# Kernel tuning notes

Hardware: AMD Instinct MI355X
Metric: run time of the kernel (lower is better)

## Reference

```python
import jax, jax.numpy as jnp
import numpy as np
from jax import lax

D_MODEL = 512
D_INNER = 1024   # expand=2
D_STATE = 16
D_CONV = 4
DT_RANK = 32     # ceil(d_model/16)
D_FFN = 2048
EPS = 1e-6


def _layernorm(x, g, b):
    mu = jnp.mean(x, axis=-1, keepdims=True)
    var = jnp.mean((x - mu) ** 2, axis=-1, keepdims=True)
    return (x - mu) * lax.rsqrt(var + EPS) * g + b


def _mamba(x, in_w, conv_w, conv_b, xproj_w, dt_w, dt_b, A_log, D_vec, out_w):
    # x: [B, L, d_model]
    B, L, _ = x.shape
    xz = jnp.einsum('bld,ed->ble', x, in_w)           # [B, L, 2*d_inner]
    xc, z = xz[..., :D_INNER], xz[..., D_INNER:]
    # causal depthwise conv over time
    xt = xc.transpose(0, 2, 1)                        # [B, d_inner, L]
    kern = conv_w[:, None, :]                         # [d_inner, 1, d_conv]
    xt = lax.conv_general_dilated(xt, kern, (1,), [(D_CONV - 1, 0)],
                                  feature_group_count=D_INNER)
    xc = jax.nn.silu(xt.transpose(0, 2, 1) + conv_b)  # [B, L, d_inner]
    # input-dependent SSM parameters
    x_dbl = jnp.einsum('bld,ed->ble', xc, xproj_w)    # [B, L, dt_rank+2*d_state]
    dt = x_dbl[..., :DT_RANK]
    Bm = x_dbl[..., DT_RANK:DT_RANK + D_STATE]
    Cm = x_dbl[..., DT_RANK + D_STATE:]
    delta = jax.nn.softplus(jnp.einsum('blr,dr->bld', dt, dt_w) + dt_b)  # [B, L, d_inner]
    A = -jnp.exp(A_log)                               # [d_inner, d_state]

    def step(h, inp):
        d_t, u_t, b_t, c_t = inp                      # [B,di],[B,di],[B,ds],[B,ds]
        dA = jnp.exp(d_t[:, :, None] * A)             # [B, di, ds]
        dBu = (d_t * u_t)[:, :, None] * b_t[:, None, :]
        h = dA * h + dBu
        y = jnp.einsum('bds,bs->bd', h, c_t)
        return h, y

    h0 = jnp.zeros((B, D_INNER, D_STATE), x.dtype)
    xs = (delta.transpose(1, 0, 2), xc.transpose(1, 0, 2),
          Bm.transpose(1, 0, 2), Cm.transpose(1, 0, 2))
    _, ys = lax.scan(step, h0, xs)                    # [L, B, d_inner]
    y = ys.transpose(1, 0, 2) + xc * D_vec
    y = y * jax.nn.silu(z)
    return jnp.einsum('ble,de->bld', y, out_w)        # [B, L, d_model]


def setup_inputs() -> dict:
    key = jax.random.key(0)
    ks = iter(jax.random.split(key, 40))
    B, S, T = 8, 512, 1024

    def nrm(shape, scale=0.02):
        return jax.random.normal(next(ks), shape, dtype=jnp.float32) * scale

    def mamba_params(prefix):
        A_log = jnp.log(jnp.broadcast_to(jnp.arange(1, D_STATE + 1, dtype=jnp.float32),
                                         (D_INNER, D_STATE)))
        return {
            prefix + '_in_w': nrm((2 * D_INNER, D_MODEL)),
            prefix + '_conv_w': nrm((D_INNER, D_CONV), 0.1),
            prefix + '_conv_b': jnp.zeros((D_INNER,), jnp.float32),
            prefix + '_xproj_w': nrm((DT_RANK + 2 * D_STATE, D_INNER)),
            prefix + '_dt_w': nrm((D_INNER, DT_RANK), 0.1),
            prefix + '_dt_b': jnp.full((D_INNER,), -4.0, jnp.float32),
            prefix + '_A_log': A_log,
            prefix + '_D_vec': jnp.ones((D_INNER,), jnp.float32),
            prefix + '_out_w': nrm((D_MODEL, D_INNER)),
        }

    inp = {
        'tgt': jax.random.normal(next(ks), (B, S, D_MODEL), dtype=jnp.float32),
        'memory': jax.random.normal(next(ks), (B, T, D_MODEL), dtype=jnp.float32),
    }
    inp.update(mamba_params('self'))
    inp.update(mamba_params('cross'))
    inp.update({
        'ln1_g': jnp.ones((D_MODEL,), jnp.float32), 'ln1_b': jnp.zeros((D_MODEL,), jnp.float32),
        'ln2_g': jnp.ones((D_MODEL,), jnp.float32), 'ln2_b': jnp.zeros((D_MODEL,), jnp.float32),
        'ln3_g': jnp.ones((D_MODEL,), jnp.float32), 'ln3_b': jnp.zeros((D_MODEL,), jnp.float32),
        'ffn_w1': nrm((D_FFN, D_MODEL)), 'ffn_b1': jnp.zeros((D_FFN,), jnp.float32),
        'ffn_w2': nrm((D_MODEL, D_FFN)), 'ffn_b2': jnp.zeros((D_MODEL,), jnp.float32),
    })
    return inp


def reference(tgt, memory,
              self_in_w, self_conv_w, self_conv_b, self_xproj_w, self_dt_w, self_dt_b,
              self_A_log, self_D_vec, self_out_w,
              cross_in_w, cross_conv_w, cross_conv_b, cross_xproj_w, cross_dt_w, cross_dt_b,
              cross_A_log, cross_D_vec, cross_out_w,
              ln1_g, ln1_b, ln2_g, ln2_b, ln3_g, ln3_b,
              ffn_w1, ffn_b1, ffn_w2, ffn_b2):
    S = tgt.shape[1]
    # self-Mamba block (post-norm, dropout=0)
    t2 = _mamba(tgt, self_in_w, self_conv_w, self_conv_b, self_xproj_w,
                self_dt_w, self_dt_b, self_A_log, self_D_vec, self_out_w)
    t = _layernorm(tgt + t2, ln1_g, ln1_b)
    # cross-Mamba: scan over [memory; tgt], keep last S steps
    cat = jnp.concatenate([memory, t], axis=1)
    c2 = _mamba(cat, cross_in_w, cross_conv_w, cross_conv_b, cross_xproj_w,
                cross_dt_w, cross_dt_b, cross_A_log, cross_D_vec, cross_out_w)[:, -S:]
    t = _layernorm(t + c2, ln2_g, ln2_b)
    # positionwise FFN
    f = jnp.einsum('bld,fd->blf', t, ffn_w1) + ffn_b1
    f = jax.nn.relu(f)
    f = jnp.einsum('blf,df->bld', f, ffn_w2) + ffn_b2
    t = _layernorm(t + f, ln3_g, ln3_b)
    return t
```

## Files before the change

kernel.cpp:

```cpp
#include <hip/hip_runtime.h>
#include <math.h>

#define DM    512
#define DI    1024
#define DSN   16
#define DTR   32
#define DFFN  2048
#define BB    8
#define SS    512
#define TTM   1024
#define LCAT  1536
#define NC    64

#define ACT_NONE     0
#define ACT_RELU     1
#define ACT_DELTA    3
#define ACT_XDBL     4

typedef __attribute__((ext_vector_type(8))) short short8;
typedef __attribute__((ext_vector_type(8))) unsigned short ushort8;
typedef __attribute__((ext_vector_type(4))) float f32x4;

#define L2E 1.4426950408889634f

__device__ __forceinline__ unsigned short f2b(float f) {
    unsigned int u = __float_as_uint(f);
    return (unsigned short)((u + 0x7FFFu + ((u >> 16) & 1u)) >> 16);
}
__device__ __forceinline__ float b2f(unsigned short h) {
    return __uint_as_float(((unsigned int)h) << 16);
}
__device__ __forceinline__ float fast_softplus(float v) {
    return (v > 20.f) ? v : __logf(1.f + __expf(v));
}
__device__ __forceinline__ float fexp2(float x) {
#if __has_builtin(__builtin_amdgcn_exp2f)
    return __builtin_amdgcn_exp2f(x);
#else
    float r; asm("v_exp_f32 %0, %1" : "=v"(r) : "v"(x)); return r;
#endif
}
__device__ __forceinline__ float frcp(float x) {
    return __builtin_amdgcn_rcpf(x);
}
__device__ __forceinline__ void gld16(const void* g, void* l) {
    __builtin_amdgcn_global_load_lds(
        (const __attribute__((address_space(1))) void*)g,
        (__attribute__((address_space(3))) void*)l, 16, 0, 0);
}

__device__ __forceinline__ int map_row(int m, int mb, int bs, int ro) {
    int q = m / mb;
    return q * bs + ro + (m - q * mb);
}

__global__ __launch_bounds__(256) void mgemm_kernel(
    const unsigned short* __restrict__ A, int mb, int bs, int ro,
    const unsigned short* __restrict__ W, const float* __restrict__ bias,
    float* __restrict__ Cf, unsigned short* __restrict__ Cb,
    float* __restrict__ C2, float* __restrict__ Cf2,
    int N, int K, int act)
{
    __shared__ __align__(16) unsigned short As[128 * 64];
    __shared__ __align__(16) unsigned short Bs[128 * 64];
    int tid = threadIdx.x;
    int lane = tid & 63, wave = tid >> 6;
    int wy = wave >> 1, wx = wave & 1;
    int nx = gridDim.x;
    int f = blockIdx.y * nx + blockIdx.x;
    int xcd = f & 7, j2 = f >> 3;
    int bandh = gridDim.y >> 3;
    int m0 = (xcd * bandh + j2 / nx) * 128;
    int n0 = (j2 % nx) * 128;
    int Kh = K / gridDim.z;
    int kbeg = blockIdx.z * Kh, kend = kbeg + Kh;
    float* Cfo = Cf;
    const float* biaso = bias;
    if (blockIdx.z) { Cfo = Cf2; biaso = nullptr; }

    const unsigned short* ga[4];
    const unsigned short* gb[4];
    unsigned short* la[4];
    unsigned short* lb[4];
    #pragma unroll
    for (int j = 0; j < 4; j++) {
        int c  = wave * 256 + j * 64 + lane;
        int r  = c >> 3;
        int q  = c & 7;
        int g  = (q & 4) | ((q & 3) ^ (r & 3));
        int arow = map_row(m0 + r, mb, bs, ro);
        ga[j] = A + (size_t)arow * K + g * 8;
        gb[j] = W + (size_t)(n0 + r) * K + g * 8;
        la[j] = As + (size_t)(wave * 256 + j * 64) * 8;
        lb[j] = Bs + (size_t)(wave * 256 + j * 64) * 8;
    }
    int fm = lane & 15, fg = lane >> 4;
    int sw = fg ^ (fm & 3);
    const unsigned short* arp = As + ((size_t)(wy * 64 + fm) * 8 + sw) * 8;
    const unsigned short* brp = Bs + ((size_t)(wx * 64 + fm) * 8 + sw) * 8;

    f32x4 acc[4][4];
    #pragma unroll
    for (int i = 0; i < 4; i++)
        #pragma unroll
        for (int j = 0; j < 4; j++) acc[i][j] = 0.f;

    for (int k0 = kbeg; k0 < kend; k0 += 64) {
        #pragma unroll
        for (int j = 0; j < 4; j++) {
            gld16(ga[j] + k0, la[j]);
            gld16(gb[j] + k0, lb[j]);
        }
        __syncthreads();
        #pragma unroll
        for (int h = 0; h < 2; h++) {
            short8 af[4], bfr[4];
            #pragma unroll
            for (int t = 0; t < 4; t++) af[t]  = *(const short8*)(arp + h * 32 + t * 1024);
            #pragma unroll
            for (int t = 0; t < 4; t++) bfr[t] = *(const short8*)(brp + h * 32 + t * 1024);
            #pragma unroll
            for (int i = 0; i < 4; i++)
                #pragma unroll
                for (int j = 0; j < 4; j++)
                    acc[i][j] = __builtin_amdgcn_mfma_f32_16x16x32_bf16(af[i], bfr[j], acc[i][j], 0, 0, 0);
        }
        __syncthreads();
    }

    int en = lane & 15, em = (lane >> 4) * 4;
    if (act == ACT_XDBL) {
        #pragma unroll
        for (int j = 0; j < 4; j++) {
            int n = n0 + wx * 64 + j * 16 + en;
            if (n >= 64) continue;
            #pragma unroll
            for (int i = 0; i < 4; i++) {
                int mbase = m0 + wy * 64 + i * 16 + em;
                #pragma unroll
                for (int r = 0; r < 4; r++) {
                    float v = acc[i][j][r];
                    int m = mbase + r;
                    if (n < 32) {
                        Cb[(size_t)m * 64 + n] = f2b(v);
                    } else {
                        C2[(size_t)m * 32 + (n - 32)] = v;
                        Cb[(size_t)m * 64 + n] = 0;
                    }
                }
            }
        }
        return;
    }
    if (act == ACT_DELTA) {
        #pragma unroll
        for (int j = 0; j < 4; j++) {
            int n = n0 + wx * 64 + j * 16 + en;
            float bv = bias[n];
            #pragma unroll
            for (int i = 0; i < 4; i++) {
                int mbase = m0 + wy * 64 + i * 16 + em;
                #pragma unroll
                for (int r = 0; r < 4; r++) {
                    float v = acc[i][j][r] + bv;
                    Cb[(size_t)(mbase + r) * 1024 + n] = f2b(fast_softplus(v));
                }
            }
        }
        return;
    }
    #pragma unroll
    for (int j = 0; j < 4; j++) {
        int n = n0 + wx * 64 + j * 16 + en;
        float bv = biaso ? biaso[n] : 0.f;
        #pragma unroll
        for (int i = 0; i < 4; i++) {
            int mbase = m0 + wy * 64 + i * 16 + em;
            #pragma unroll
            for (int r = 0; r < 4; r++) {
                float v = acc[i][j][r] + bv;
                if (act == ACT_RELU) v = v > 0.f ? v : 0.f;
                size_t off = (size_t)(mbase + r) * N + n;
                if (Cb) Cb[off] = f2b(v);
                else    Cfo[off] = v;
            }
        }
    }
}

__global__ void xprojb_fill(const float* __restrict__ xproj, unsigned short* __restrict__ out)
{
    int idx = blockIdx.x * 256 + threadIdx.x;
    if (idx >= 131072) return;
    int n = idx >> 10;
    out[idx] = (n < 64) ? f2b(xproj[idx]) : (unsigned short)0;
}
__global__ void dtwb_fill(const float* __restrict__ dt_w, unsigned short* __restrict__ out)
{
    int idx = blockIdx.x * 256 + threadIdx.x;
    if (idx >= 65536) return;
    int n = idx >> 6, c = idx & 63;
    out[idx] = (c < 32) ? f2b(dt_w[n * 32 + c]) : (unsigned short)0;
}

__global__ __launch_bounds__(256) void conv_silu_kernel(
    const unsigned short* __restrict__ xz,
    const float* __restrict__ cw,
    const float* __restrict__ cb,
    unsigned short* __restrict__ xc, int L, int total8)
{
    int idx = blockIdx.x * blockDim.x + threadIdx.x;
    if (idx >= total8) return;
    int d8 = idx & 127;
    int d0 = d8 * 8;
    int r  = idx >> 7;
    int l  = r % L;
    float acc[8];
    {
        float4 c0 = ((const float4*)(cb + d0))[0];
        float4 c1 = ((const float4*)(cb + d0))[1];
        acc[0]=c0.x; acc[1]=c0.y; acc[2]=c0.z; acc[3]=c0.w;
        acc[4]=c1.x; acc[5]=c1.y; acc[6]=c1.z; acc[7]=c1.w;
    }
    float4 wv[8];
    #pragma unroll
    for (int j = 0; j < 8; j++) wv[j] = *(const float4*)(cw + (d0 + j) * 4);
    #pragma unroll
    for (int k = 0; k < 4; k++) {
        int ls = l - 3 + k;
        if (ls >= 0) {
            ushort8 v = *(const ushort8*)(xz + (size_t)(r - 3 + k) * 2048 + d0);
            const float* w = (const float*)&wv[0];
            #pragma unroll
            for (int j = 0; j < 8; j++)
                acc[j] = fmaf(b2f(v[j]), w[j * 4 + k], acc[j]);
        }
    }
    ushort8 o;
    #pragma unroll
    for (int j = 0; j < 8; j++) {
        float s = acc[j] * frcp(1.f + __expf(-acc[j]));
        o[j] = f2b(s);
    }
    *(ushort8*)(xc + (size_t)r * 1024 + d0) = o;
}

__global__ __launch_bounds__(256) void scan_part1(
    const unsigned short* __restrict__ delta, const unsigned short* __restrict__ xc,
    const float* __restrict__ bc, const float* __restrict__ A_log,
    float* __restrict__ part_h, float* __restrict__ part_s, int L, int CH)
{
    int tid = threadIdx.x;
    int dblk = blockIdx.x & 3;
    int c    = (blockIdx.x >> 2) & (NC - 1);
    int b    = blockIdx.x / (4 * NC);
    int d    = dblk * 256 + tid;
    float A2[DSN];
    {
        const float4* ap = (const float4*)(A_log + d * DSN);
        #pragma unroll
        for (int q = 0; q < 4; q++) {
            float4 a4 = ap[q];
            A2[q*4+0] = -__expf(a4.x) * L2E;
            A2[q*4+1] = -__expf(a4.y) * L2E;
            A2[q*4+2] = -__expf(a4.z) * L2E;
            A2[q*4+3] = -__expf(a4.w) * L2E;
        }
    }
    float h[DSN];
    #pragma unroll
    for (int s = 0; s < DSN; s++) h[s] = 0.f;
    float ssum = 0.f;
    int l0 = c * CH;
    for (int l = l0; l < l0 + CH; l++) {
        size_t r = (size_t)b * L + l;
        float4 bq[4];
        const float4* bp = (const float4*)(bc + r * 32);
        #pragma unroll
        for (int q = 0; q < 4; q++) bq[q] = bp[q];
        const float* Bm = (const float*)&bq[0];
        float dl = b2f(delta[r * DI + d]);
        float u  = b2f(xc[r * DI + d]);
        float du = dl * u;
        ssum += dl;
        #pragma unroll
        for (int s = 0; s < DSN; s++)
            h[s] = fmaf(fexp2(dl * A2[s]), h[s], du * Bm[s]);
    }
    size_t base = ((size_t)(b * NC + c) * DI + d) * DSN;
    #pragma unroll
    for (int q = 0; q < 4; q++)
        ((float4*)(part_h + base))[q] = make_float4(h[q*4], h[q*4+1], h[q*4+2], h[q*4+3]);
    part_s[(size_t)(b * NC + c) * DI + d] = ssum;
}

__global__ __launch_bounds__(256) void scan_combine(
    const float* __restrict__ A_log,
    float* __restrict__ part_h, const float* __restrict__ part_s)
{
    int idx = blockIdx.x * 256 + threadIdx.x;
    int s  = idx & (DSN - 1);
    int dd = (idx >> 4) & (DI - 1);
    int b  = idx >> 14;
    float A2 = -__expf(A_log[dd * DSN + s]) * L2E;
    float h = 0.f;
    size_t sbase = (size_t)b * NC * DI + dd;
    size_t hbase = ((size_t)b * NC * DI + dd) * DSN + s;
    for (int c = 0; c < NC; c++) {
        float ph = part_h[hbase];
        float S  = part_s[sbase];
        part_h[hbase] = h;
        h = fmaf(fexp2(A2 * S), h, ph);
        hbase += (size_t)DI * DSN;
        sbase += DI;
    }
}

__global__ __launch_bounds__(256) void scan_part2(
    const unsigned short* __restrict__ delta, const unsigned short* __restrict__ xc,
    const float* __restrict__ bc, const unsigned short* __restrict__ xz,
    const float* __restrict__ A_log, const float* __restrict__ Dv,
    const float* __restrict__ part_h,
    unsigned short* __restrict__ out, int L, int CH)
{
    int tid = threadIdx.x;
    int dblk = blockIdx.x & 3;
    int c    = (blockIdx.x >> 2) & (NC - 1);
    int b    = blockIdx.x / (4 * NC);
    int d    = dblk * 256 + tid;
    float A2[DSN];
    {
        const float4* ap = (const float4*)(A_log + d * DSN);
        #pragma unroll
        for (int q = 0; q < 4; q++) {
            float4 a4 = ap[q];
            A2[q*4+0] = -__expf(a4.x) * L2E;
            A2[q*4+1] = -__expf(a4.y) * L2E;
            A2[q*4+2] = -__expf(a4.z) * L2E;
            A2[q*4+3] = -__expf(a4.w) * L2E;
        }
    }
    float Dvd = Dv[d];
    size_t base = ((size_t)(b * NC + c) * DI + d) * DSN;
    float h4[4][4];
    #pragma unroll
    for (int q = 0; q < 4; q++) *((float4*)h4[q]) = ((const float4*)(part_h + base))[q];
    float h[DSN];
    #pragma unroll
    for (int s = 0; s < DSN; s++) h[s] = h4[s >> 2][s & 3];
    int l0 = c * CH;
    for (int l = l0; l < l0 + CH; l++) {
        size_t r = (size_t)b * L + l;
        float4 bq[8];
        const float4* bp = (const float4*)(bc + r * 32);
        #pragma unroll
        for (int q = 0; q < 8; q++) bq[q] = bp[q];
        const float* Bm = (const float*)&bq[0];
        const float* Cm = Bm + DSN;
        float dl = b2f(delta[r * DI + d]);
        float u  = b2f(xc[r * DI + d]);
        float du = dl * u;
        float y = 0.f;
        #pragma unroll
        for (int s = 0; s < DSN; s++) {
            h[s] = fmaf(fexp2(dl * A2[s]), h[s], du * Bm[s]);
            y = fmaf(h[s], Cm[s], y);
        }
        float z = b2f(xz[r * 2048 + DI + d]);
        float sil = z * frcp(1.f + __expf(-z));
        out[r * DI + d] = f2b((y + u * Dvd) * sil);
    }
}

__global__ __launch_bounds__(128) void addln_kernel(
    const float* __restrict__ a, int amb, int absd, int aro, int lda,
    const float* __restrict__ bsrc, const float* __restrict__ bsrc2,
    const float* __restrict__ g, const float* __restrict__ be,
    float* __restrict__ outf, int omb, int obsd, int oro, int ldo,
    unsigned short* __restrict__ outb, int bmb, int bbsd, int bro, int ldb)
{
    int m = blockIdx.x, t = threadIdx.x;
    int ar = map_row(m, amb, absd, aro);
    float4 x4 = ((const float4*)(a + (size_t)ar * lda))[t];
    float4 y4 = ((const float4*)(bsrc + (size_t)m * DM))[t];
    float v[4] = {x4.x + y4.x, x4.y + y4.y, x4.z + y4.z, x4.w + y4.w};
    if (bsrc2) {
        float4 z4 = ((const float4*)(bsrc2 + (size_t)m * DM))[t];
        v[0] += z4.x; v[1] += z4.y; v[2] += z4.z; v[3] += z4.w;
    }
    float sum = v[0] + v[1] + v[2] + v[3];
    float sq  = v[0]*v[0] + v[1]*v[1] + v[2]*v[2] + v[3]*v[3];
    #pragma unroll
    for (int o = 32; o > 0; o >>= 1) {
        sum += __shfl_down(sum, o);
        sq  += __shfl_down(sq, o);
    }
    __shared__ float s0[2], s1[2];
    if ((t & 63) == 0) { s0[t >> 6] = sum; s1[t >> 6] = sq; }
    __syncthreads();
    float tot = s0[0] + s0[1];
    float tsq = s1[0] + s1[1];
    float mu = tot * (1.f / DM);
    float var = tsq * (1.f / DM) - mu * mu;
    float rs = rsqrtf(var + 1e-6f);
    float4 g4 = ((const float4*)g)[t];
    float4 b4 = ((const float4*)be)[t];
    float o0 = (v[0] - mu) * rs * g4.x + b4.x;
    float o1 = (v[1] - mu) * rs * g4.y + b4.y;
    float o2 = (v[2] - mu) * rs * g4.z + b4.z;
    float o3 = (v[3] - mu) * rs * g4.w + b4.w;
    if (outf) {
        int orow = map_row(m, omb, obsd, oro);
        ((float4*)(outf + (size_t)orow * ldo))[t] = make_float4(o0, o1, o2, o3);
    }
    if (outb) {
        int brow = map_row(m, bmb, bbsd, bro);
        ((ushort4*)(outb + (size_t)brow * ldb))[t] =
            make_ushort4(f2b(o0), f2b(o1), f2b(o2), f2b(o3));
    }
}

__global__ void f2b_kernel(const float* __restrict__ in, unsigned short* __restrict__ out, int n4)
{
    int i = blockIdx.x * 256 + threadIdx.x;
    if (i >= n4) return;
    float4 v = ((const float4*)in)[i];
    ((ushort4*)out)[i] = make_ushort4(f2b(v.x), f2b(v.y), f2b(v.z), f2b(v.w));
}

struct W6 { const float* p[6]; };
__global__ void wconv_kernel(W6 w, unsigned short* __restrict__ out)
{
    const int cum[7] = {0, 262144, 524288, 655360, 786432, 1048576, 1310720};
    int i = blockIdx.x * 256 + threadIdx.x;
    if (i >= 1310720) return;
    int seg = 0;
    #pragma unroll
    for (int s = 1; s < 6; s++) seg += (i >= cum[s]);
    float4 v = ((const float4*)w.p[seg])[i - cum[seg]];
    ((ushort4*)out)[i] = make_ushort4(f2b(v.x), f2b(v.y), f2b(v.z), f2b(v.w));
}

__global__ void mem2catb_kernel(const float* __restrict__ mem, unsigned short* __restrict__ catb)
{
    int f = blockIdx.x * blockDim.x + threadIdx.x;
    const int total = BB * TTM * DM / 4;
    if (f >= total) return;
    const int per_b = TTM * DM / 4;
    int b = f / per_b, rem = f - b * per_b;
    float4 v = ((const float4*)mem)[f];
    ((ushort4*)catb)[(size_t)b * (LCAT * DM / 4) + rem] =
        make_ushort4(f2b(v.x), f2b(v.y), f2b(v.z), f2b(v.w));
}

static void run_scan(const unsigned short* dltb, const unsigned short* xcb, const float* bc,
                     const unsigned short* xzb, const float* A_log, const float* Dv,
                     float* part_h, float* part_s, unsigned short* out, int L,
                     hipStream_t stream)
{
    int CH = L / NC;
    int blocks = BB * NC * (DI / 256);
    scan_part1<<<blocks, 256, 0, stream>>>(dltb, xcb, bc, A_log, part_h, part_s, L, CH);
    scan_combine<<<BB * DI * DSN / 256, 256, 0, stream>>>(A_log, part_h, part_s);
    scan_part2<<<blocks, 256, 0, stream>>>(dltb, xcb, bc, xzb, A_log, Dv, part_h, out, L, CH);
}

extern "C" void kernel_launch(void* const* d_in, const int* in_sizes, int n_in,
                              void* d_out, int out_size, void* d_ws, size_t ws_size,
                              hipStream_t stream)
{
    const float* tgt       = (const float*)d_in[0];
    const float* memory    = (const float*)d_in[1];
    const float* s_in_w    = (const float*)d_in[2];
    const float* s_conv_w  = (const float*)d_in[3];
    const float* s_conv_b  = (const float*)d_in[4];
    const float* s_xproj_w = (const float*)d_in[5];
    const float* s_dt_w    = (const float*)d_in[6];
    const float* s_dt_b    = (const float*)d_in[7];
    const float* s_A_log   = (const float*)d_in[8];
    const float* s_D_vec   = (const float*)d_in[9];
    const float* s_out_w   = (const float*)d_in[10];
    const float* c_in_w    = (const float*)d_in[11];
    const float* c_conv_w  = (const float*)d_in[12];
    const float* c_conv_b  = (const float*)d_in[13];
    const float* c_xproj_w = (const float*)d_in[14];
    const float* c_dt_w    = (const float*)d_in[15];
    const float* c_dt_b    = (const float*)d_in[16];
    const float* c_A_log   = (const float*)d_in[17];
    const float* c_D_vec   = (const float*)d_in[18];
    const float* c_out_w   = (const float*)d_in[19];
    const float* ln1_g     = (const float*)d_in[20];
    const float* ln1_b     = (const float*)d_in[21];
    const float* ln2_g     = (const float*)d_in[22];
    const float* ln2_b     = (const float*)d_in[23];
    const float* ln3_g     = (const float*)d_in[24];
    const float* ln3_b     = (const float*)d_in[25];
    const float* ffn_w1    = (const float*)d_in[26];
    const float* ffn_b1    = (const float*)d_in[27];
    const float* ffn_w2    = (const float*)d_in[28];
    const float* ffn_b2    = (const float*)d_in[29];
    float* outp = (float*)d_out;

    float* ws     = (float*)d_ws;
    float* bc     = ws;
    float* t1     = bc     + 393216;
    float* tbuf   = t1     + 2097152;
    float* part_h = tbuf   + 2097152;
    float* proj   = part_h;
    float* proj2  = part_h + 2097152;
    float* part_s = part_h + 8388608;
    unsigned short* ub      = (unsigned short*)(part_s + 524288);
    unsigned short* dltb    = ub;
    unsigned short* catb    = dltb    + 12582912;
    unsigned short* tgtb    = catb    + 6291456;
    unsigned short* xzb     = tgtb    + 2097152;
    unsigned short* xcb     = xzb     + 25165824;
    unsigned short* ygb     = xcb     + 12582912;
    unsigned short* tbbf    = ygb     + 12582912;
    unsigned short* s_in_wb = tbbf    + 2097152;
    unsigned short* c_in_wb = s_in_wb + 1048576;
    unsigned short* s_out_wb= c_in_wb + 1048576;
    unsigned short* c_out_wb= s_out_wb+ 524288;
    unsigned short* w1b     = c_out_wb+ 524288;
    unsigned short* w2b     = w1b     + 1048576;
    unsigned short* xprojb_s= w2b     + 1048576;
    unsigned short* xprojb_c= xprojb_s+ 131072;
    unsigned short* dtwb_s  = xprojb_c+ 131072;
    unsigned short* dtwb_c  = dtwb_s  + 65536;
    unsigned short* dtb     = dtwb_c  + 65536;
    unsigned short* fbuf    = xzb;
    float* ffnout  = (float*)dltb;
    float* ffnout2 = ffnout + 2097152;

    f2b_kernel<<<(2097152/4 + 255)/256, 256, 0, stream>>>(tgt, tgtb, 2097152/4);
    mem2catb_kernel<<<(BB*TTM*DM/4 + 255)/256, 256, 0, stream>>>(memory, catb);
    {
        W6 w; w.p[0]=s_in_w; w.p[1]=c_in_w; w.p[2]=s_out_w; w.p[3]=c_out_w; w.p[4]=ffn_w1; w.p[5]=ffn_w2;
        wconv_kernel<<<(1310720 + 255)/256, 256, 0, stream>>>(w, s_in_wb);
    }
    xprojb_fill<<<131072/256, 256, 0, stream>>>(s_xproj_w, xprojb_s);
    xprojb_fill<<<131072/256, 256, 0, stream>>>(c_xproj_w, xprojb_c);
    dtwb_fill<<<65536/256, 256, 0, stream>>>(s_dt_w, dtwb_s);
    dtwb_fill<<<65536/256, 256, 0, stream>>>(c_dt_w, dtwb_c);

    mgemm_kernel<<<dim3(2048/128, 4096/128), 256, 0, stream>>>(
        tgtb, 4096, 0, 0, s_in_wb, nullptr, nullptr, xzb, nullptr, nullptr, 2048, 512, ACT_NONE);
    conv_silu_kernel<<<(BB*SS*DI/8 + 255)/256, 256, 0, stream>>>(xzb, s_conv_w, s_conv_b, xcb, SS, BB*SS*DI/8);
    mgemm_kernel<<<dim3(1, 4096/128), 256, 0, stream>>>(
        xcb, 4096, 0, 0, xprojb_s, nullptr, nullptr, dtb, bc, nullptr, 128, 1024, ACT_XDBL);
    mgemm_kernel<<<dim3(1024/128, 4096/128), 256, 0, stream>>>(
        dtb, 4096, 0, 0, dtwb_s, s_dt_b, nullptr, dltb, nullptr, nullptr, 1024, 64, ACT_DELTA);
    run_scan(dltb, xcb, bc, xzb, s_A_log, s_D_vec, part_h, part_s, ygb, SS, stream);
    mgemm_kernel<<<dim3(512/128, 4096/128, 2), 256, 0, stream>>>(
        ygb, 4096, 0, 0, s_out_wb, nullptr, proj, nullptr, nullptr, proj2, 512, 1024, ACT_NONE);
    addln_kernel<<<4096, 128, 0, stream>>>(
        tgt, 4096, 0, 0, DM, proj, proj2, ln1_g, ln1_b,
        t1, 4096, 0, 0, DM, catb, 512, 1536, 1024, DM);

    mgemm_kernel<<<dim3(2048/128, 12288/128), 256, 0, stream>>>(
        catb, 12288, 0, 0, c_in_wb, nullptr, nullptr, xzb, nullptr, nullptr, 2048, 512, ACT_NONE);
    conv_silu_kernel<<<(BB*LCAT*DI/8 + 255)/256, 256, 0, stream>>>(xzb, c_conv_w, c_conv_b, xcb, LCAT, BB*LCAT*DI/8);
    mgemm_kernel<<<dim3(1, 12288/128), 256, 0, stream>>>(
        xcb, 12288, 0, 0, xprojb_c, nullptr, nullptr, dtb, bc, nullptr, 128, 1024, ACT_XDBL);
    mgemm_kernel<<<dim3(1024/128, 12288/128), 256, 0, stream>>>(
        dtb, 12288, 0, 0, dtwb_c, c_dt_b, nullptr, dltb, nullptr, nullptr, 1024, 64, ACT_DELTA);
    run_scan(dltb, xcb, bc, xzb, c_A_log, c_D_vec, part_h, part_s, ygb, LCAT, stream);
    mgemm_kernel<<<dim3(512/128, 4096/128, 2), 256, 0, stream>>>(
        ygb, 512, 1536, 1024, c_out_wb, nullptr, proj, nullptr, nullptr, proj2, 512, 1024, ACT_NONE);
    addln_kernel<<<4096, 128, 0, stream>>>(
        t1, 4096, 0, 0, DM, proj, proj2, ln2_g, ln2_b,
        tbuf, 4096, 0, 0, DM, tbbf, 4096, 0, 0, DM);

    mgemm_kernel<<<dim3(2048/128, 4096/128), 256, 0, stream>>>(
        tbbf, 4096, 0, 0, w1b, ffn_b1, nullptr, fbuf, nullptr, nullptr, 2048, 512, ACT_RELU);
    mgemm_kernel<<<dim3(512/128, 4096/128, 2), 256, 0, stream>>>(
        fbuf, 4096, 0, 0, w2b, ffn_b2, ffnout, nullptr, nullptr, ffnout2, 512, 2048, ACT_NONE);
    addln_kernel<<<4096, 128, 0, stream>>>(
        tbuf, 4096, 0, 0, DM, ffnout, ffnout2, ln3_g, ln3_b,
        outp, 4096, 0, 0, DM, nullptr, 0, 0, 0, 0);
}
```

Before: 591.5 us.

## Skip unneeded cross-Mamba z projection and scan output for memory rows

The cross-Mamba in-projection is split in two. The x half is computed for all concatenated rows, and the z (gate) half is computed only for the last 512 rows per batch, using a new row-mapped output addressing in the GEMM. The scan's second pass now launches only the chunks that cover the kept tail (from chunk 42 on) and writes gated outputs only for positions at or after 1024. This removes GEMM and scan work whose results are discarded by the final slice, at the cost of an extra GEMM launch and some index arithmetic in the epilogue.

Measured after the change: 581.3 us. About the same (-1.7%).

```diff
diff --git a/kernel.cpp b/kernel.cpp
--- a/kernel.cpp
+++ b/kernel.cpp
@@ -59,7 +59,8 @@
     const unsigned short* __restrict__ W, const float* __restrict__ bias,
     float* __restrict__ Cf, unsigned short* __restrict__ Cb,
     float* __restrict__ C2, float* __restrict__ Cf2,
-    int N, int K, int act)
+    int N, int K, int act,
+    int omb, int obs, int oro, int ldc, int nofs)
 {
     __shared__ __align__(16) unsigned short As[128 * 64];
     __shared__ __align__(16) unsigned short Bs[128 * 64];
@@ -180,7 +181,8 @@
             for (int r = 0; r < 4; r++) {
                 float v = acc[i][j][r] + bv;
                 if (act == ACT_RELU) v = v > 0.f ? v : 0.f;
-                size_t off = (size_t)(mbase + r) * N + n;
+                int orow = map_row(mbase + r, omb, obs, oro);
+                size_t off = (size_t)orow * ldc + nofs + n;
                 if (Cb) Cb[off] = f2b(v);
                 else    Cfo[off] = v;
             }
@@ -321,12 +323,14 @@
     const float* __restrict__ bc, const unsigned short* __restrict__ xz,
     const float* __restrict__ A_log, const float* __restrict__ Dv,
     const float* __restrict__ part_h,
-    unsigned short* __restrict__ out, int L, int CH)
+    unsigned short* __restrict__ out, int L, int CH, int c0, int lmin)
 {
     int tid = threadIdx.x;
     int dblk = blockIdx.x & 3;
-    int c    = (blockIdx.x >> 2) & (NC - 1);
-    int b    = blockIdx.x / (4 * NC);
+    int rest = blockIdx.x >> 2;
+    int ncp  = NC - c0;
+    int c    = c0 + rest % ncp;
+    int b    = rest / ncp;
     int d    = dblk * 256 + tid;
     float A2[DSN];
     {
@@ -366,9 +370,11 @@
             h[s] = fmaf(fexp2(dl * A2[s]), h[s], du * Bm[s]);
             y = fmaf(h[s], Cm[s], y);
         }
-        float z = b2f(xz[r * 2048 + DI + d]);
-        float sil = z * frcp(1.f + __expf(-z));
-        out[r * DI + d] = f2b((y + u * Dvd) * sil);
+        if (l >= lmin) {
+            float z = b2f(xz[r * 2048 + DI + d]);
+            float sil = z * frcp(1.f + __expf(-z));
+            out[r * DI + d] = f2b((y + u * Dvd) * sil);
+        }
     }
 }
 
@@ -456,13 +462,14 @@
 static void run_scan(const unsigned short* dltb, const unsigned short* xcb, const float* bc,
                      const unsigned short* xzb, const float* A_log, const float* Dv,
                      float* part_h, float* part_s, unsigned short* out, int L,
-                     hipStream_t stream)
+                     int c0, int lmin, hipStream_t stream)
 {
     int CH = L / NC;
-    int blocks = BB * NC * (DI / 256);
-    scan_part1<<<blocks, 256, 0, stream>>>(dltb, xcb, bc, A_log, part_h, part_s, L, CH);
+    int blocks1 = BB * NC * (DI / 256);
+    scan_part1<<<blocks1, 256, 0, stream>>>(dltb, xcb, bc, A_log, part_h, part_s, L, CH);
     scan_combine<<<BB * DI * DSN / 256, 256, 0, stream>>>(A_log, part_h, part_s);
-    scan_part2<<<blocks, 256, 0, stream>>>(dltb, xcb, bc, xzb, A_log, Dv, part_h, out, L, CH);
+    int blocks2 = BB * (NC - c0) * (DI / 256);
+    scan_part2<<<blocks2, 256, 0, stream>>>(dltb, xcb, bc, xzb, A_log, Dv, part_h, out, L, CH, c0, lmin);
 }
 
 extern "C" void kernel_launch(void* const* d_in, const int* in_sizes, int n_in,
@@ -544,37 +551,50 @@
     dtwb_fill<<<65536/256, 256, 0, stream>>>(c_dt_w, dtwb_c);
 
     mgemm_kernel<<<dim3(2048/128, 4096/128), 256, 0, stream>>>(
-        tgtb, 4096, 0, 0, s_in_wb, nullptr, nullptr, xzb, nullptr, nullptr, 2048, 512, ACT_NONE);
+        tgtb, 4096, 0, 0, s_in_wb, nullptr, nullptr, xzb, nullptr, nullptr, 2048, 512, ACT_NONE,
+        4096, 0, 0, 2048, 0);
     conv_silu_kernel<<<(BB*SS*DI/8 + 255)/256, 256, 0, stream>>>(xzb, s_conv_w, s_conv_b, xcb, SS, BB*SS*DI/8);
     mgemm_kernel<<<dim3(1, 4096/128), 256, 0, stream>>>(
-        xcb, 4096, 0, 0, xprojb_s, nullptr, nullptr, dtb, bc, nullptr, 128, 1024, ACT_XDBL);
+        xcb, 4096, 0, 0, xprojb_s, nullptr, nullptr, dtb, bc, nullptr, 128, 1024, ACT_XDBL,
+        4096, 0, 0, 128, 0);
     mgemm_kernel<<<dim3(1024/128, 4096/128), 256, 0, stream>>>(
-        dtb, 4096, 0, 0, dtwb_s, s_dt_b, nullptr, dltb, nullptr, nullptr, 1024, 64, ACT_DELTA);
-    run_scan(dltb, xcb, bc, xzb, s_A_log, s_D_vec, part_h, part_s, ygb, SS, stream);
+        dtb, 4096, 0, 0, dtwb_s, s_dt_b, nullptr, dltb, nullptr, nullptr, 1024, 64, ACT_DELTA,
+        4096, 0, 0, 1024, 0);
+    run_scan(dltb, xcb, bc, xzb, s_A_log, s_D_vec, part_h, part_s, ygb, SS, 0, 0, stream);
     mgemm_kernel<<<dim3(512/128, 4096/128, 2), 256, 0, stream>>>(
-        ygb, 4096, 0, 0, s_out_wb, nullptr, proj, nullptr, nullptr, proj2, 512, 1024, ACT_NONE);
+        ygb, 4096, 0, 0, s_out_wb, nullptr, proj, nullptr, nullptr, proj2, 512, 1024, ACT_NONE,
+        4096, 0, 0, 512, 0);
     addln_kernel<<<4096, 128, 0, stream>>>(
         tgt, 4096, 0, 0, DM, proj, proj2, ln1_g, ln1_b,
         t1, 4096, 0, 0, DM, catb, 512, 1536, 1024, DM);
 
-    mgemm_kernel<<<dim3(2048/128, 12288/128), 256, 0, stream>>>(
-        catb, 12288, 0, 0, c_in_wb, nullptr, nullptr, xzb, nullptr, nullptr, 2048, 512, ACT_NONE);
+    mgemm_kernel<<<dim3(1024/128, 12288/128), 256, 0, stream>>>(
+        catb, 12288, 0, 0, c_in_wb, nullptr, nullptr, xzb, nullptr, nullptr, 2048, 512, ACT_NONE,
+        12288, 0, 0, 2048, 0);
+    mgemm_kernel<<<dim3(1024/128, 4096/128), 256, 0, stream>>>(
+        catb, 512, 1536, 1024, c_in_wb + 1024 * 512, nullptr, nullptr, xzb, nullptr, nullptr, 2048, 512, ACT_NONE,
+        512, 1536, 1024, 2048, 1024);
     conv_silu_kernel<<<(BB*LCAT*DI/8 + 255)/256, 256, 0, stream>>>(xzb, c_conv_w, c_conv_b, xcb, LCAT, BB*LCAT*DI/8);
     mgemm_kernel<<<dim3(1, 12288/128), 256, 0, stream>>>(
-        xcb, 12288, 0, 0, xprojb_c, nullptr, nullptr, dtb, bc, nullptr, 128, 1024, ACT_XDBL);
+        xcb, 12288, 0, 0, xprojb_c, nullptr, nullptr, dtb, bc, nullptr, 128, 1024, ACT_XDBL,
+        12288, 0, 0, 128, 0);
     mgemm_kernel<<<dim3(1024/128, 12288/128), 256, 0, stream>>>(
-        dtb, 12288, 0, 0, dtwb_c, c_dt_b, nullptr, dltb, nullptr, nullptr, 1024, 64, ACT_DELTA);
-    run_scan(dltb, xcb, bc, xzb, c_A_log, c_D_vec, part_h, part_s, ygb, LCAT, stream);
+        dtb, 12288, 0, 0, dtwb_c, c_dt_b, nullptr, dltb, nullptr, nullptr, 1024, 64, ACT_DELTA,
+        12288, 0, 0, 1024, 0);
+    run_scan(dltb, xcb, bc, xzb, c_A_log, c_D_vec, part_h, part_s, ygb, LCAT, 42, 1024, stream);
     mgemm_kernel<<<dim3(512/128, 4096/128, 2), 256, 0, stream>>>(
-        ygb, 512, 1536, 1024, c_out_wb, nullptr, proj, nullptr, nullptr, proj2, 512, 1024, ACT_NONE);
+        ygb, 512, 1536, 1024, c_out_wb, nullptr, proj, nullptr, nullptr, proj2, 512, 1024, ACT_NONE,
+        4096, 0, 0, 512, 0);
     addln_kernel<<<4096, 128, 0, stream>>>(
         t1, 4096, 0, 0, DM, proj, proj2, ln2_g, ln2_b,
         tbuf, 4096, 0, 0, DM, tbbf, 4096, 0, 0, DM);
 
     mgemm_kernel<<<dim3(2048/128, 4096/128), 256, 0, stream>>>(
-        tbbf, 4096, 0, 0, w1b, ffn_b1, nullptr, fbuf, nullptr, nullptr, 2048, 512, ACT_RELU);
+        tbbf, 4096, 0, 0, w1b, ffn_b1, nullptr, fbuf, nullptr, nullptr, 2048, 512, ACT_RELU,
+        4096, 0, 0, 2048, 0);
     mgemm_kernel<<<dim3(512/128, 4096/128, 2), 256, 0, stream>>>(
-        fbuf, 4096, 0, 0, w2b, ffn_b2, ffnout, nullptr, nullptr, ffnout2, 512, 2048, ACT_NONE);
+        fbuf, 4096, 0, 0, w2b, ffn_b2, ffnout, nullptr, nullptr, ffnout2, 512, 2048, ACT_NONE,
+        4096, 0, 0, 512, 0);
     addln_kernel<<<4096, 128, 0, stream>>>(
         tbuf, 4096, 0, 0, DM, ffnout, ffnout2, ln3_g, ln3_b,
         outp, 4096, 0, 0, DM, nullptr, 0, 0, 0, 0);
```
